# Optimization experiments

Hardware: AMD Instinct MI355X
Metric: run time of the kernel (lower is better)

Reference implementation:

```python
import jax, jax.numpy as jnp
import numpy as np

N, E, B, L, D, H = 50000, 800000, 64, 32, 256, 256


def setup_inputs() -> dict:
    key = jax.random.key(0)
    ks = jax.random.split(key, 20)
    s = 0.05
    inp = {
        'x': jax.random.normal(ks[0], (N, D), jnp.float32),
        'edge_index': jax.random.randint(ks[1], (2, E), 0, N),
        'batch': jnp.sort(jax.random.randint(ks[2], (N,), 0, B)),
        'paths': jax.random.randint(ks[3], (B, L), 0, N),
        # SAGEConv1: lin_l (aggregated neighbors, with bias) + lin_r (root, no bias)
        'w1l': jax.random.normal(ks[4], (D, H), jnp.float32) * s,
        'b1l': jnp.zeros((H,), jnp.float32),
        'w1r': jax.random.normal(ks[5], (D, H), jnp.float32) * s,
        # SAGEConv2
        'w2l': jax.random.normal(ks[6], (H, H), jnp.float32) * s,
        'b2l': jnp.zeros((H,), jnp.float32),
        'w2r': jax.random.normal(ks[7], (H, H), jnp.float32) * s,
        # LSTM (gate order i,f,g,o as in torch)
        'w_ih': jax.random.normal(ks[8], (4 * H, H), jnp.float32) * s,
        'w_hh': jax.random.normal(ks[9], (4 * H, H), jnp.float32) * s,
        'b_ih': jnp.zeros((4 * H,), jnp.float32),
        'b_hh': jnp.zeros((4 * H,), jnp.float32),
        # scorer MLP
        'wm1': jax.random.normal(ks[10], (2 * H, H), jnp.float32) * s,
        'bm1': jnp.zeros((H,), jnp.float32),
        'wm2': jax.random.normal(ks[11], (H, 1), jnp.float32) * s,
        'bm2': jnp.zeros((1,), jnp.float32),
    }
    return inp


def sage_conv(x, src, dst, wl, bl, wr):
    # mean-aggregate neighbor features (messages flow src -> dst)
    agg = jax.ops.segment_sum(x[src], dst, num_segments=N)
    deg = jax.ops.segment_sum(jnp.ones((src.shape[0],), x.dtype), dst, num_segments=N)
    mean = agg / jnp.maximum(deg, 1.0)[:, None]
    return mean @ wl + bl + x @ wr


def lstm_last_hidden(seq, w_ih, w_hh, b_ih, b_hh):
    # seq: [B, L, H] -> hn: [B, H]
    h0 = jnp.zeros((seq.shape[0], H), seq.dtype)
    c0 = jnp.zeros_like(h0)

    def step(carry, xt):
        h, c = carry
        gates = xt @ w_ih.T + b_ih + h @ w_hh.T + b_hh
        i, f, g, o = jnp.split(gates, 4, axis=-1)
        c = jax.nn.sigmoid(f) * c + jax.nn.sigmoid(i) * jnp.tanh(g)
        h = jax.nn.sigmoid(o) * jnp.tanh(c)
        return (h, c), None

    (hn, _), _ = jax.lax.scan(step, (h0, c0), jnp.swapaxes(seq, 0, 1))
    return hn


def reference(x, edge_index, batch, paths, w1l, b1l, w1r, w2l, b2l, w2r,
              w_ih, w_hh, b_ih, b_hh, wm1, bm1, wm2, bm2):
    src, dst = edge_index[0], edge_index[1]
    h = jax.nn.relu(sage_conv(x, src, dst, w1l, b1l, w1r))
    node_emb = sage_conv(h, src, dst, w2l, b2l, w2r)  # [N, H]

    # global mean pool per graph
    gsum = jax.ops.segment_sum(node_emb, batch, num_segments=B)
    gcnt = jax.ops.segment_sum(jnp.ones((N,), node_emb.dtype), batch, num_segments=B)
    graph_emb = gsum / jnp.maximum(gcnt, 1.0)[:, None]  # [B, H]

    path_seq = node_emb[paths]  # [B, L, H]
    path_emb = lstm_last_hidden(path_seq, w_ih, w_hh, b_ih, b_hh)  # [B, H]

    combined = jnp.concatenate([graph_emb, path_emb], axis=-1)  # [B, 2H]
    scores = jax.nn.relu(combined @ wm1 + bm1) @ wm2 + bm2  # [B, 1]
    return scores.reshape(-1)  # torch.cat of per-path [1] scores -> [B]
```

## Files before the change

### kernel.cpp

```cpp
#include <hip/hip_runtime.h>

namespace {

constexpr int NN = 50000;
constexpr int NE = 800000;
constexpr int NB = 64;
constexpr int NL = 32;
constexpr int ND = 256;
constexpr int NSCAN = 196;

typedef __attribute__((ext_vector_type(8))) short short8v;
typedef __attribute__((ext_vector_type(4))) float float4v;

__device__ __forceinline__ float sigf(float x){ return 1.0f/(1.0f + __expf(-x)); }

__device__ __forceinline__ void split8(float4 fa, float4 fb, uint4& h, uint4& lo){
  uint a0=__float_as_uint(fa.x), a1=__float_as_uint(fa.y), a2=__float_as_uint(fa.z), a3=__float_as_uint(fa.w);
  uint b0=__float_as_uint(fb.x), b1=__float_as_uint(fb.y), b2=__float_as_uint(fb.z), b3=__float_as_uint(fb.w);
  h.x = (a0>>16) | (a1 & 0xFFFF0000u);
  h.y = (a2>>16) | (a3 & 0xFFFF0000u);
  h.z = (b0>>16) | (b1 & 0xFFFF0000u);
  h.w = (b2>>16) | (b3 & 0xFFFF0000u);
  float r0 = fa.x - __uint_as_float(a0 & 0xFFFF0000u);
  float r1 = fa.y - __uint_as_float(a1 & 0xFFFF0000u);
  float r2 = fa.z - __uint_as_float(a2 & 0xFFFF0000u);
  float r3 = fa.w - __uint_as_float(a3 & 0xFFFF0000u);
  float r4 = fb.x - __uint_as_float(b0 & 0xFFFF0000u);
  float r5 = fb.y - __uint_as_float(b1 & 0xFFFF0000u);
  float r6 = fb.z - __uint_as_float(b2 & 0xFFFF0000u);
  float r7 = fb.w - __uint_as_float(b3 & 0xFFFF0000u);
  lo.x = (__float_as_uint(r0)>>16) | (__float_as_uint(r1) & 0xFFFF0000u);
  lo.y = (__float_as_uint(r2)>>16) | (__float_as_uint(r3) & 0xFFFF0000u);
  lo.z = (__float_as_uint(r4)>>16) | (__float_as_uint(r5) & 0xFFFF0000u);
  lo.w = (__float_as_uint(r6)>>16) | (__float_as_uint(r7) & 0xFFFF0000u);
}

__global__ void k_hist(const int* __restrict__ dst, int* __restrict__ cnt){
  int stride = gridDim.x * blockDim.x;
  for (int e = blockIdx.x*blockDim.x + threadIdx.x; e < NE; e += stride)
    atomicAdd(&cnt[dst[e]], 1);
}

__global__ void k_scan_block(const int* __restrict__ cnt, int* __restrict__ offs,
                             int* __restrict__ bsum){
  __shared__ int s[256];
  const int t = threadIdx.x, i = blockIdx.x*256 + t;
  int v = cnt[i];
  s[t] = v; __syncthreads();
  #pragma unroll
  for (int off = 1; off < 256; off <<= 1){
    int x = (t >= off) ? s[t-off] : 0;
    __syncthreads();
    s[t] += x;
    __syncthreads();
  }
  offs[i] = s[t] - v;
  if (t == 255) bsum[blockIdx.x] = s[255];
}

__global__ void k_scan_top(const int* __restrict__ bsum, int* __restrict__ bsum2){
  __shared__ int s[256];
  const int t = threadIdx.x;
  int v = (t < NSCAN) ? bsum[t] : 0;
  s[t] = v; __syncthreads();
  #pragma unroll
  for (int off = 1; off < 256; off <<= 1){
    int x = (t >= off) ? s[t-off] : 0;
    __syncthreads();
    s[t] += x;
    __syncthreads();
  }
  if (t < NSCAN) bsum2[t] = s[t] - v;
}

__global__ void k_scan_add(int* __restrict__ offs, const int* __restrict__ bsum2,
                           int* __restrict__ cursor){
  const int i = blockIdx.x*256 + threadIdx.x;
  int v = offs[i] + bsum2[blockIdx.x];
  offs[i] = v;
  cursor[i] = v;
}

__global__ void k_fill(const int* __restrict__ src, const int* __restrict__ dst,
                       int* __restrict__ cursor, int* __restrict__ csr){
  int stride = gridDim.x * blockDim.x;
  for (int e = blockIdx.x*blockDim.x + threadIdx.x; e < NE; e += stride){
    int d = dst[e];
    int pos = atomicAdd(&cursor[d], 1);
    csr[pos] = src[e];
  }
}

__launch_bounds__(256, 8)
__global__ void k_gather(const float* __restrict__ feat, const int* __restrict__ offs,
                         const int* __restrict__ csr, float* __restrict__ out){
  __shared__ float4 sp[256];
  const int u = blockIdx.x, t = threadIdx.x;
  const int w = t >> 6, l = t & 63;
  const int beg = offs[u], end = offs[u+1];
  const int lc = l * 4;
  float a0 = 0.f, a1 = 0.f, a2 = 0.f, a3 = 0.f;
  int e = beg + w;
  for (; e + 4 < end; e += 8){
    int s0 = csr[e], s1 = csr[e+4];
    const float4 v0 = *(const float4*)(feat + (long long)s0*ND + lc);
    const float4 v1 = *(const float4*)(feat + (long long)s1*ND + lc);
    a0 += v0.x + v1.x; a1 += v0.y + v1.y; a2 += v0.z + v1.z; a3 += v0.w + v1.w;
  }
  if (e < end){
    int s0 = csr[e];
    const float4 v0 = *(const float4*)(feat + (long long)s0*ND + lc);
    a0 += v0.x; a1 += v0.y; a2 += v0.z; a3 += v0.w;
  }
  sp[t] = make_float4(a0, a1, a2, a3);
  __syncthreads();
  if (t < 64){
    float4 p0 = sp[t], p1 = sp[64+t], p2 = sp[128+t], p3 = sp[192+t];
    float inv = 1.0f / fmaxf((float)(end - beg), 1.0f);
    float4 r;
    r.x = (p0.x + p1.x + p2.x + p3.x) * inv;
    r.y = (p0.y + p1.y + p2.y + p3.y) * inv;
    r.z = (p0.z + p1.z + p2.z + p3.z) * inv;
    r.w = (p0.w + p1.w + p2.w + p3.w) * inv;
    *(float4*)(out + (long long)u*ND + t*4) = r;
  }
}

__global__ void k_wsplit(const float* __restrict__ wl, const float* __restrict__ wr,
                         ushort* __restrict__ WtH, ushort* __restrict__ WtL){
  const int k = blockIdx.x;
  const int n = threadIdx.x;
  float v = (k < 256) ? wl[k*256 + n] : wr[(k-256)*256 + n];
  uint u = __float_as_uint(v);
  float r = v - __uint_as_float(u & 0xFFFF0000u);
  const int wc = n >> 6, nt = (n >> 4) & 3, lm = n & 15;
  const int kk = k >> 5, lq = (k >> 3) & 3, j = k & 7;
  const long long idx = (long long)(((wc*4 + nt)*16 + kk)*64 + lq*16 + lm)*8 + j;
  WtH[idx] = (ushort)(u >> 16);
  WtL[idx] = (ushort)(__float_as_uint(r) >> 16);
}

__launch_bounds__(256, 2)
__global__ void k_gemm_mfma(const float* __restrict__ A1, const float* __restrict__ A2,
                            const ushort* __restrict__ WtH, const ushort* __restrict__ WtL,
                            const float* __restrict__ bias, float* __restrict__ C, int relu)
{
  __shared__ float eb[16*260];
  const int t  = threadIdx.x;
  const int w  = t >> 6;
  const int l  = t & 63;
  const int lm = l & 15;
  const int lq = l >> 4;
  const int m0 = blockIdx.x * 64;

  const uint4* BH4 = (const uint4*)WtH;
  const uint4* BL4 = (const uint4*)WtL;

  const float4v vzero = {0.f, 0.f, 0.f, 0.f};
  float4v acc[4][4];
  #pragma unroll
  for (int i = 0; i < 4; ++i)
    #pragma unroll
    for (int j = 0; j < 4; ++j) acc[i][j] = vzero;

  long long arow[4];
  #pragma unroll
  for (int mt = 0; mt < 4; ++mt){
    int row = m0 + mt*16 + lm;
    row = (row < NN) ? row : (NN - 1);
    arow[mt] = (long long)row * ND;
  }
  int bbase[4];
  #pragma unroll
  for (int nt = 0; nt < 4; ++nt) bbase[nt] = (w*4 + nt)*1024 + l;

  auto ldB = [&](int kk, uint4* bh, uint4* bl){
    #pragma unroll
    for (int nt = 0; nt < 4; ++nt){
      int idx = bbase[nt] + kk*64;
      bh[nt] = BH4[idx];
      bl[nt] = BL4[idx];
    }
  };
  auto ldA = [&](int kk, uint4* ah, uint4* al){
    const float* Ab = (kk < 8) ? A1 : A2;
    const int koff = (kk & 7)*32 + lq*8;
    #pragma unroll
    for (int mt = 0; mt < 4; ++mt){
      const float* p = Ab + arow[mt] + koff;
      float4 fa = *(const float4*)p;
      float4 fb = *(const float4*)(p + 4);
      split8(fa, fb, ah[mt], al[mt]);
    }
  };

  uint4 bhb[2][4], blb[2][4], ahb[2][4], alb[2][4];
  ldB(0, bhb[0], blb[0]);
  ldA(0, ahb[0], alb[0]);

  #pragma unroll
  for (int kk = 0; kk < 16; ++kk){
    const int cur = kk & 1, nx = cur ^ 1;
    if (kk < 15){
      ldB(kk + 1, bhb[nx], blb[nx]);
      ldA(kk + 1, ahb[nx], alb[nx]);
    }
    #pragma unroll
    for (int nt = 0; nt < 4; ++nt){
      short8v bh = *(short8v*)&bhb[cur][nt];
      short8v bl = *(short8v*)&blb[cur][nt];
      #pragma unroll
      for (int mt = 0; mt < 4; ++mt){
        short8v ah = *(short8v*)&ahb[cur][mt];
        short8v al = *(short8v*)&alb[cur][mt];
        acc[mt][nt] = __builtin_amdgcn_mfma_f32_16x16x32_bf16(ah, bh, acc[mt][nt], 0, 0, 0);
        acc[mt][nt] = __builtin_amdgcn_mfma_f32_16x16x32_bf16(al, bh, acc[mt][nt], 0, 0, 0);
        acc[mt][nt] = __builtin_amdgcn_mfma_f32_16x16x32_bf16(ah, bl, acc[mt][nt], 0, 0, 0);
      }
    }
  }

  float bvv[4];
  #pragma unroll
  for (int nt = 0; nt < 4; ++nt) bvv[nt] = bias[w*64 + nt*16 + lm];

  #pragma unroll
  for (int mt = 0; mt < 4; ++mt){
    #pragma unroll
    for (int nt = 0; nt < 4; ++nt){
      #pragma unroll
      for (int r = 0; r < 4; ++r){
        float v = acc[mt][nt][r] + bvv[nt];
        if (relu) v = fmaxf(v, 0.f);
        eb[(lq*4 + r)*260 + w*64 + nt*16 + lm] = v;
      }
    }
    __syncthreads();
    #pragma unroll
    for (int i = 0; i < 4; ++i){
      int idx = i*256 + t;
      int rr  = idx >> 6;
      int c4  = (idx & 63) * 4;
      int grow = m0 + mt*16 + rr;
      if (grow < NN)
        *(float4*)(C + (long long)grow*ND + c4) = *(float4*)&eb[rr*260 + c4];
    }
    __syncthreads();
  }
}

__launch_bounds__(256, 3)
__global__ void k_xgate(const float* __restrict__ emb, const int* __restrict__ paths,
                        const float* __restrict__ w_ih, const float* __restrict__ b_ih,
                        const float* __restrict__ b_hh, float* __restrict__ xg)
{
  __shared__ float As[16][68];
  __shared__ float Ws[16][260];
  const int t  = threadIdx.x;
  const int m0 = blockIdx.x * 64;
  const int g0 = blockIdx.y * 256;
  const int rg = t >> 5, cg = t & 31;
  const int sm = t >> 2, sj = (t & 3) * 4;

  float acc[8][8];
  #pragma unroll
  for (int i = 0; i < 8; ++i)
    #pragma unroll
    for (int j = 0; j < 8; ++j) acc[i][j] = 0.f;

  const int node = paths[m0 + sm];
  const float* arow = emb  + (long long)node*ND;
  const float* wrow = w_ih + (long long)(g0 + t)*ND;

  for (int k0 = 0; k0 < 256; k0 += 16){
    float4 av = *(const float4*)(arow + k0 + sj);
    float4 q0 = *(const float4*)(wrow + k0 + 0);
    float4 q1 = *(const float4*)(wrow + k0 + 4);
    float4 q2 = *(const float4*)(wrow + k0 + 8);
    float4 q3 = *(const float4*)(wrow + k0 + 12);
    __syncthreads();
    As[sj+0][sm]=av.x; As[sj+1][sm]=av.y; As[sj+2][sm]=av.z; As[sj+3][sm]=av.w;
    Ws[ 0][t]=q0.x; Ws[ 1][t]=q0.y; Ws[ 2][t]=q0.z; Ws[ 3][t]=q0.w;
    Ws[ 4][t]=q1.x; Ws[ 5][t]=q1.y; Ws[ 6][t]=q1.z; Ws[ 7][t]=q1.w;
    Ws[ 8][t]=q2.x; Ws[ 9][t]=q2.y; Ws[10][t]=q2.z; Ws[11][t]=q2.w;
    Ws[12][t]=q3.x; Ws[13][t]=q3.y; Ws[14][t]=q3.z; Ws[15][t]=q3.w;
    __syncthreads();
    #pragma unroll
    for (int k = 0; k < 16; ++k){
      float a[8], b[8];
      *(float4*)&a[0] = *(const float4*)&As[k][rg*8];
      *(float4*)&a[4] = *(const float4*)&As[k][rg*8+4];
      *(float4*)&b[0] = *(const float4*)&Ws[k][cg*8];
      *(float4*)&b[4] = *(const float4*)&Ws[k][cg*8+4];
      #pragma unroll
      for (int i = 0; i < 8; ++i)
        #pragma unroll
        for (int j = 0; j < 8; ++j)
          acc[i][j] = fmaf(a[i], b[j], acc[i][j]);
    }
  }

  float bv[8];
  #pragma unroll
  for (int j = 0; j < 8; ++j){ int g = g0 + cg*8 + j; bv[j] = b_ih[g] + b_hh[g]; }
  #pragma unroll
  for (int i = 0; i < 8; ++i){
    int row = m0 + rg*8 + i;
    float o[8];
    #pragma unroll
    for (int j = 0; j < 8; ++j) o[j] = acc[i][j] + bv[j];
    *(float4*)(xg + (long long)row*1024 + g0 + cg*8 + 0) = *(float4*)&o[0];
    *(float4*)(xg + (long long)row*1024 + g0 + cg*8 + 4) = *(float4*)&o[4];
  }
}

__launch_bounds__(256, 4)
__global__ void k_lstm_step(const float* __restrict__ h_in, float* __restrict__ h_out,
                            float* __restrict__ c_state, const float* __restrict__ xg,
                            const float* __restrict__ w_hh, int tstep)
{
  __shared__ float ws[4*256];
  __shared__ float hs[32*260];
  __shared__ float part[2*128];
  __shared__ float gs[128];
  const int t  = threadIdx.x;
  const int u  = blockIdx.x >> 1;
  const int b0 = (blockIdx.x & 1) * 32;

  {
    int gate = t >> 6, c4 = (t & 63) * 4;
    float4 v = *(const float4*)(w_hh + (long long)(gate*256 + u)*256 + c4);
    *(float4*)&ws[gate*256 + c4] = v;
  }
  #pragma unroll
  for (int i = 0; i < 8; ++i){
    int idx = i*256 + t;
    int b = idx >> 6, c4 = (idx & 63) * 4;
    float4 v = *(const float4*)(h_in + (long long)(b0 + b)*256 + c4);
    *(float4*)&hs[b*260 + c4] = v;
  }
  __syncthreads();

  const int b  = t & 31;
  const int g  = (t >> 5) & 3;
  const int kd = t >> 7;
  float s = 0.f;
  const float* hp = &hs[b*260 + kd*128];
  const float* wp = &ws[g*256 + kd*128];
  #pragma unroll
  for (int k4 = 0; k4 < 32; ++k4){
    float4 h4 = *(const float4*)(hp + k4*4);
    float4 w4 = *(const float4*)(wp + k4*4);
    s += h4.x*w4.x + h4.y*w4.y + h4.z*w4.z + h4.w*w4.w;
  }
  part[kd*128 + b*4 + g] = s;
  __syncthreads();

  if (t < 128){
    int bb = t >> 2, gg = t & 3;
    const float* xp = xg + ((long long)(b0 + bb)*NL + tstep)*1024;
    gs[t] = part[t] + part[128 + t] + xp[gg*256 + u];
  }
  __syncthreads();

  if (t < 32){
    float gi = gs[t*4+0], gf = gs[t*4+1], gG = gs[t*4+2], go = gs[t*4+3];
    int bb = b0 + t;
    float c_old = c_state[bb*256 + u];
    float c_new = sigf(gf)*c_old + sigf(gi)*tanhf(gG);
    c_state[bb*256 + u] = c_new;
    h_out[bb*256 + u] = sigf(go)*tanhf(c_new);
  }
}

__global__ void k_pool(const float* __restrict__ emb, const int* __restrict__ batch,
                       float* __restrict__ gsum, float* __restrict__ gcnt)
{
  __shared__ int bs[256];
  const int t  = threadIdx.x;
  const int n0 = blockIdx.x * 256;
  {
    int n = n0 + t;
    bs[t] = (n < NN) ? batch[n] : -1;
  }
  __syncthreads();
  int cur = bs[0];
  float acc = 0.f; int cnt = 0;
  for (int j = 0; j < 256; ++j){
    int nn = n0 + j;
    if (nn >= NN) break;
    int g = bs[j];
    if (g != cur){
      unsafeAtomicAdd(&gsum[cur*256 + t], acc);
      if (t == 0) unsafeAtomicAdd(&gcnt[cur], (float)cnt);
      acc = 0.f; cnt = 0; cur = g;
    }
    acc += emb[(long long)nn*256 + t];
    ++cnt;
  }
  if (cnt > 0 && cur >= 0){
    unsafeAtomicAdd(&gsum[cur*256 + t], acc);
    if (t == 0) unsafeAtomicAdd(&gcnt[cur], (float)cnt);
  }
}

__global__ void k_score(const float* __restrict__ gsum, const float* __restrict__ gcnt,
                        const float* __restrict__ hfin, const float* __restrict__ wm1,
                        const float* __restrict__ bm1, const float* __restrict__ wm2,
                        const float* __restrict__ bm2, float* __restrict__ out)
{
  __shared__ float cs[512];
  __shared__ float red[4];
  const int b = blockIdx.x, t = threadIdx.x;
  float inv = 1.0f / fmaxf(gcnt[b], 1.0f);
  cs[t]       = gsum[b*256 + t] * inv;
  cs[256 + t] = hfin[b*256 + t];
  __syncthreads();
  float v = 0.f;
  #pragma unroll 4
  for (int k = 0; k < 512; ++k) v = fmaf(cs[k], wm1[(long long)k*256 + t], v);
  v = fmaxf(v + bm1[t], 0.f) * wm2[t];
  #pragma unroll
  for (int off = 32; off > 0; off >>= 1) v += __shfl_down(v, off, 64);
  if ((t & 63) == 0) red[t >> 6] = v;
  __syncthreads();
  if (t == 0) out[b] = red[0] + red[1] + red[2] + red[3] + bm2[0];
}

}

extern "C" void kernel_launch(void* const* d_in, const int* in_sizes, int n_in,
                              void* d_out, int out_size, void* d_ws, size_t ws_size,
                              hipStream_t stream)
{
  const float* x     = (const float*)d_in[0];
  const int*   eidx  = (const int*)  d_in[1];
  const int*   batch = (const int*)  d_in[2];
  const int*   paths = (const int*)  d_in[3];
  const float* w1l   = (const float*)d_in[4];
  const float* b1l   = (const float*)d_in[5];
  const float* w1r   = (const float*)d_in[6];
  const float* w2l   = (const float*)d_in[7];
  const float* b2l   = (const float*)d_in[8];
  const float* w2r   = (const float*)d_in[9];
  const float* w_ih  = (const float*)d_in[10];
  const float* w_hh  = (const float*)d_in[11];
  const float* b_ih  = (const float*)d_in[12];
  const float* b_hh  = (const float*)d_in[13];
  const float* wm1   = (const float*)d_in[14];
  const float* bm1   = (const float*)d_in[15];
  const float* wm2   = (const float*)d_in[16];
  const float* bm2   = (const float*)d_in[17];

  const int* src = eidx;
  const int* dst = eidx + NE;

  float* w    = (float*)d_ws;
  float* bufA = w;
  float* bufB = bufA + (long long)NN*ND;
  float* xg   = bufB + (long long)NN*ND;
  float* gsum = xg   + 2048*1024;
  float* gcnt = gsum + NB*ND;
  float* h0   = gcnt + 64;
  float* c0   = h0   + NB*ND;
  float* h1   = c0   + NB*ND;
  ushort* wt1H = (ushort*)(h1 + NB*ND);
  ushort* wt1L = wt1H + 256*512;
  ushort* wt2H = wt1L + 256*512;
  ushort* wt2L = wt2H + 256*512;

  int* cnt    = (int*)xg;
  int* offs   = cnt    + 50432;
  int* cursor = offs   + 50432;
  int* bsum   = cursor + 50432;
  int* bsum2  = bsum   + 256;
  int* csr    = bsum2  + 256;

  k_wsplit<<<512, 256, 0, stream>>>(w1l, w1r, wt1H, wt1L);
  k_wsplit<<<512, 256, 0, stream>>>(w2l, w2r, wt2H, wt2L);

  hipMemsetAsync(cnt, 0, 50432*sizeof(int), stream);
  k_hist<<<1024, 256, 0, stream>>>(dst, cnt);
  k_scan_block<<<NSCAN, 256, 0, stream>>>(cnt, offs, bsum);
  k_scan_top<<<1, 256, 0, stream>>>(bsum, bsum2);
  k_scan_add<<<NSCAN, 256, 0, stream>>>(offs, bsum2, cursor);
  k_fill<<<1024, 256, 0, stream>>>(src, dst, cursor, csr);

  k_gather<<<NN, 256, 0, stream>>>(x, offs, csr, bufA);
  k_gemm_mfma<<<(NN+63)/64, 256, 0, stream>>>(bufA, x, wt1H, wt1L, b1l, bufB, 1);

  k_gather<<<NN, 256, 0, stream>>>(bufB, offs, csr, bufA);
  k_gemm_mfma<<<(NN+63)/64, 256, 0, stream>>>(bufA, bufB, wt2H, wt2L, b2l, bufA, 0);

  hipMemsetAsync(gsum, 0, (NB*ND + 64)*sizeof(float), stream);
  k_pool<<<(NN+255)/256, 256, 0, stream>>>(bufA, batch, gsum, gcnt);

  k_xgate<<<dim3((NB*NL)/64, 1024/256), 256, 0, stream>>>(bufA, paths, w_ih, b_ih, b_hh, xg);

  hipMemsetAsync(h0, 0, 2*(size_t)NB*ND*sizeof(float), stream);
  for (int ts = 0; ts < NL; ++ts){
    float* hin  = (ts & 1) ? h1 : h0;
    float* hout = (ts & 1) ? h0 : h1;
    k_lstm_step<<<512, 256, 0, stream>>>(hin, hout, c0, xg, w_hh, ts);
  }

  k_score<<<NB, 256, 0, stream>>>(gsum, gcnt, h0, wm1, bm1, wm2, bm2, (float*)d_out);
}
```

Before: 941.6 us.

## Fuse LSTM timesteps into one cooperative persistent kernel with split-bf16 MFMA

Replaces the 32 per-timestep LSTM kernel launches with a single cooperative kernel of 64 blocks. Each block keeps its slice of w_hh in shared memory as hi/lo bf16 pairs and computes the recurrent matvec with three bf16 MFMAs per k-step. Timesteps are separated by a grid-wide sync, and the cell state stays in registers. This removes per-step launch overhead and the repeated reload of w_hh, in exchange for grid barrier latency and a small precision loss from the bf16 split.

```diff
diff --git a/kernel.cpp b/kernel.cpp
--- a/kernel.cpp
+++ b/kernel.cpp
@@ -1,4 +1,7 @@
 #include <hip/hip_runtime.h>
+#include <hip/hip_cooperative_groups.h>
+
+namespace cg = cooperative_groups;
 
 namespace {
 
@@ -314,62 +317,94 @@
   }
 }
 
-__launch_bounds__(256, 4)
-__global__ void k_lstm_step(const float* __restrict__ h_in, float* __restrict__ h_out,
-                            float* __restrict__ c_state, const float* __restrict__ xg,
-                            const float* __restrict__ w_hh, int tstep)
+__launch_bounds__(256, 1)
+__global__ void k_lstm(const float* __restrict__ xg, const float* __restrict__ w_hh,
+                       ushort* __restrict__ hH, ushort* __restrict__ hL,
+                       float* __restrict__ hfin)
 {
-  __shared__ float ws[4*256];
-  __shared__ float hs[32*260];
-  __shared__ float part[2*128];
-  __shared__ float gs[128];
+  cg::grid_group grid = cg::this_grid();
+  __shared__ ushort Bh[8*64*8];
+  __shared__ ushort Bl[8*64*8];
+  __shared__ float  Gs[4*256];
   const int t  = threadIdx.x;
-  const int u  = blockIdx.x >> 1;
-  const int b0 = (blockIdx.x & 1) * 32;
-
-  {
-    int gate = t >> 6, c4 = (t & 63) * 4;
-    float4 v = *(const float4*)(w_hh + (long long)(gate*256 + u)*256 + c4);
-    *(float4*)&ws[gate*256 + c4] = v;
-  }
-  #pragma unroll
-  for (int i = 0; i < 8; ++i){
-    int idx = i*256 + t;
-    int b = idx >> 6, c4 = (idx & 63) * 4;
-    float4 v = *(const float4*)(h_in + (long long)(b0 + b)*256 + c4);
-    *(float4*)&hs[b*260 + c4] = v;
+  const int w  = t >> 6, l = t & 63;
+  const int b  = blockIdx.x;
+  const int u0 = b*4;
+  const int lm = l & 15, lq = l >> 4;
+  const int m0w = w*16;
+
+  #pragma unroll
+  for (int i = 0; i < 16; ++i){
+    int elem = i*256 + t;
+    int n = elem >> 8;
+    int k = elem & 255;
+    float v = w_hh[((n >> 2)*256 + u0 + (n & 3))*256 + k];
+    uint uv = __float_as_uint(v);
+    float r = v - __uint_as_float(uv & 0xFFFF0000u);
+    int kk = k >> 5, lqq = (k >> 3) & 3, jj = k & 7;
+    int pos = (kk*64 + lqq*16 + n)*8 + jj;
+    Bh[pos] = (ushort)(uv >> 16);
+    Bl[pos] = (ushort)(__float_as_uint(r) >> 16);
   }
   __syncthreads();
 
-  const int b  = t & 31;
-  const int g  = (t >> 5) & 3;
-  const int kd = t >> 7;
-  float s = 0.f;
-  const float* hp = &hs[b*260 + kd*128];
-  const float* wp = &ws[g*256 + kd*128];
-  #pragma unroll
-  for (int k4 = 0; k4 < 32; ++k4){
-    float4 h4 = *(const float4*)(hp + k4*4);
-    float4 w4 = *(const float4*)(wp + k4*4);
-    s += h4.x*w4.x + h4.y*w4.y + h4.z*w4.z + h4.w*w4.w;
-  }
-  part[kd*128 + b*4 + g] = s;
-  __syncthreads();
-
-  if (t < 128){
-    int bb = t >> 2, gg = t & 3;
-    const float* xp = xg + ((long long)(b0 + bb)*NL + tstep)*1024;
-    gs[t] = part[t] + part[128 + t] + xp[gg*256 + u];
-  }
-  __syncthreads();
-
-  if (t < 32){
-    float gi = gs[t*4+0], gf = gs[t*4+1], gG = gs[t*4+2], go = gs[t*4+3];
-    int bb = b0 + t;
-    float c_old = c_state[bb*256 + u];
-    float c_new = sigf(gf)*c_old + sigf(gi)*tanhf(gG);
-    c_state[bb*256 + u] = c_new;
-    h_out[bb*256 + u] = sigf(go)*tanhf(c_new);
+  const int mb = m0w + lm;
+  const int uu = u0 + lq;
+  float c = 0.f;
+
+  float xq[4];
+  #pragma unroll
+  for (int g = 0; g < 4; ++g) xq[g] = xg[(mb*NL + 0)*1024 + g*256 + uu];
+
+  for (int ts = 0; ts < NL; ++ts){
+    const int tsn = (ts < NL-1) ? ts + 1 : ts;
+    float xqn[4];
+    #pragma unroll
+    for (int g = 0; g < 4; ++g) xqn[g] = xg[(mb*NL + tsn)*1024 + g*256 + uu];
+
+    if (ts > 0){
+      const ushort* hHp = hH + ((ts-1) & 1)*16384;
+      const ushort* hLp = hL + ((ts-1) & 1)*16384;
+      float4v acc = {0.f, 0.f, 0.f, 0.f};
+      #pragma unroll
+      for (int kk = 0; kk < 8; ++kk){
+        const int koff = kk*32 + lq*8;
+        short8v ah = *(const short8v*)(hHp + mb*256 + koff);
+        short8v al = *(const short8v*)(hLp + mb*256 + koff);
+        short8v bh = *(const short8v*)&Bh[(kk*64 + l)*8];
+        short8v bl = *(const short8v*)&Bl[(kk*64 + l)*8];
+        acc = __builtin_amdgcn_mfma_f32_16x16x32_bf16(ah, bh, acc, 0, 0, 0);
+        acc = __builtin_amdgcn_mfma_f32_16x16x32_bf16(al, bh, acc, 0, 0, 0);
+        acc = __builtin_amdgcn_mfma_f32_16x16x32_bf16(ah, bl, acc, 0, 0, 0);
+      }
+      #pragma unroll
+      for (int r = 0; r < 4; ++r)
+        Gs[w*256 + (lq*4 + r)*16 + lm] = acc[r];
+    } else {
+      #pragma unroll
+      for (int r = 0; r < 4; ++r)
+        Gs[w*256 + (lq*4 + r)*16 + lm] = 0.f;
+    }
+    __syncthreads();
+
+    float gi = Gs[w*256 + lm*16 +  0 + lq] + xq[0];
+    float gf = Gs[w*256 + lm*16 +  4 + lq] + xq[1];
+    float gg = Gs[w*256 + lm*16 +  8 + lq] + xq[2];
+    float go = Gs[w*256 + lm*16 + 12 + lq] + xq[3];
+    float c_new = sigf(gf)*c + sigf(gi)*tanhf(gg);
+    c = c_new;
+    float h = sigf(go)*tanhf(c_new);
+
+    uint hu = __float_as_uint(h);
+    float hr = h - __uint_as_float(hu & 0xFFFF0000u);
+    hH[(ts & 1)*16384 + mb*256 + uu] = (ushort)(hu >> 16);
+    hL[(ts & 1)*16384 + mb*256 + uu] = (ushort)(__float_as_uint(hr) >> 16);
+    if (ts == NL-1) hfin[mb*256 + uu] = h;
+
+    xq[0]=xqn[0]; xq[1]=xqn[1]; xq[2]=xqn[2]; xq[3]=xqn[3];
+    __threadfence();
+    grid.sync();
+    __syncthreads();
   }
 }
 
@@ -462,12 +497,12 @@
   float* gsum = xg   + 2048*1024;
   float* gcnt = gsum + NB*ND;
   float* h0   = gcnt + 64;
-  float* c0   = h0   + NB*ND;
-  float* h1   = c0   + NB*ND;
-  ushort* wt1H = (ushort*)(h1 + NB*ND);
+  ushort* wt1H = (ushort*)(h0 + NB*ND);
   ushort* wt1L = wt1H + 256*512;
   ushort* wt2H = wt1L + 256*512;
   ushort* wt2L = wt2H + 256*512;
+  ushort* hH   = wt2L + 256*512;
+  ushort* hL   = hH   + 2*NB*ND;
 
   int* cnt    = (int*)xg;
   int* offs   = cnt    + 50432;
@@ -497,11 +532,12 @@
 
   k_xgate<<<dim3((NB*NL)/64, 1024/256), 256, 0, stream>>>(bufA, paths, w_ih, b_ih, b_hh, xg);
 
-  hipMemsetAsync(h0, 0, 2*(size_t)NB*ND*sizeof(float), stream);
-  for (int ts = 0; ts < NL; ++ts){
-    float* hin  = (ts & 1) ? h1 : h0;
-    float* hout = (ts & 1) ? h0 : h1;
-    k_lstm_step<<<512, 256, 0, stream>>>(hin, hout, c0, xg, w_hh, ts);
+  {
+    const float* xg_c = xg;
+    const float* whh_c = w_hh;
+    ushort* hH_c = hH; ushort* hL_c = hL; float* h0_c = h0;
+    void* args[] = { (void*)&xg_c, (void*)&whh_c, (void*)&hH_c, (void*)&hL_c, (void*)&h0_c };
+    hipLaunchCooperativeKernel((const void*)k_lstm, dim3(64), dim3(256), args, 0, stream);
   }
 
   k_score<<<NB, 256, 0, stream>>>(gsum, gcnt, h0, wm1, bm1, wm2, bm2, (float*)d_out);
```

New measurement: 1.451 ms. +54.1%, slower.

## Gather neighbor features from bf16 copies to halve gather traffic

Applied to the files above, without the earlier changes.

Adds a kernel that converts x to bf16 with round-to-nearest-even, and makes the first GEMM also write a bf16 copy of its ReLU output. Both neighbor-mean gathers now read bf16 rows and accumulate in fp32. The aim is to halve the bytes moved by the random-access gather, which reads about 800k rows of 1KB each per layer. In exchange it adds a conversion pass and an extra bf16 write, and the aggregated neighbor features lose precision.

```diff
diff --git a/kernel.cpp b/kernel.cpp
--- a/kernel.cpp
+++ b/kernel.cpp
@@ -13,6 +13,12 @@
 typedef __attribute__((ext_vector_type(4))) float float4v;
 
 __device__ __forceinline__ float sigf(float x){ return 1.0f/(1.0f + __expf(-x)); }
+
+__device__ __forceinline__ ushort rne_bf16(float f){
+  uint u = __float_as_uint(f);
+  return (ushort)((u + 0x7FFFu + ((u >> 16) & 1u)) >> 16);
+}
+__device__ __forceinline__ float bf2f(ushort u){ return __uint_as_float((uint)u << 16); }
 
 __device__ __forceinline__ void split8(float4 fa, float4 fb, uint4& h, uint4& lo){
   uint a0=__float_as_uint(fa.x), a1=__float_as_uint(fa.y), a2=__float_as_uint(fa.z), a3=__float_as_uint(fa.w);
@@ -91,9 +97,18 @@
   }
 }
 
+__global__ void k_tobf16(const float* __restrict__ in, ushort* __restrict__ out){
+  const int i = blockIdx.x*blockDim.x + threadIdx.x;
+  const float4 a = ((const float4*)in)[i*2];
+  const float4 b = ((const float4*)in)[i*2+1];
+  ushort o[8] = { rne_bf16(a.x), rne_bf16(a.y), rne_bf16(a.z), rne_bf16(a.w),
+                  rne_bf16(b.x), rne_bf16(b.y), rne_bf16(b.z), rne_bf16(b.w) };
+  ((uint4*)out)[i] = *(uint4*)o;
+}
+
 __launch_bounds__(256, 8)
-__global__ void k_gather(const float* __restrict__ feat, const int* __restrict__ offs,
-                         const int* __restrict__ csr, float* __restrict__ out){
+__global__ void k_gather_bf16(const ushort* __restrict__ feat, const int* __restrict__ offs,
+                              const int* __restrict__ csr, float* __restrict__ out){
   __shared__ float4 sp[256];
   const int u = blockIdx.x, t = threadIdx.x;
   const int w = t >> 6, l = t & 63;
@@ -103,14 +118,17 @@
   int e = beg + w;
   for (; e + 4 < end; e += 8){
     int s0 = csr[e], s1 = csr[e+4];
-    const float4 v0 = *(const float4*)(feat + (long long)s0*ND + lc);
-    const float4 v1 = *(const float4*)(feat + (long long)s1*ND + lc);
-    a0 += v0.x + v1.x; a1 += v0.y + v1.y; a2 += v0.z + v1.z; a3 += v0.w + v1.w;
+    ushort4 v0 = *(const ushort4*)(feat + (long long)s0*ND + lc);
+    ushort4 v1 = *(const ushort4*)(feat + (long long)s1*ND + lc);
+    a0 += bf2f(v0.x) + bf2f(v1.x);
+    a1 += bf2f(v0.y) + bf2f(v1.y);
+    a2 += bf2f(v0.z) + bf2f(v1.z);
+    a3 += bf2f(v0.w) + bf2f(v1.w);
   }
   if (e < end){
     int s0 = csr[e];
-    const float4 v0 = *(const float4*)(feat + (long long)s0*ND + lc);
-    a0 += v0.x; a1 += v0.y; a2 += v0.z; a3 += v0.w;
+    ushort4 v0 = *(const ushort4*)(feat + (long long)s0*ND + lc);
+    a0 += bf2f(v0.x); a1 += bf2f(v0.y); a2 += bf2f(v0.z); a3 += bf2f(v0.w);
   }
   sp[t] = make_float4(a0, a1, a2, a3);
   __syncthreads();
@@ -143,7 +161,8 @@
 __launch_bounds__(256, 2)
 __global__ void k_gemm_mfma(const float* __restrict__ A1, const float* __restrict__ A2,
                             const ushort* __restrict__ WtH, const ushort* __restrict__ WtL,
-                            const float* __restrict__ bias, float* __restrict__ C, int relu)
+                            const float* __restrict__ bias, float* __restrict__ C,
+                            ushort* __restrict__ Cb, int relu)
 {
   __shared__ float eb[16*260];
   const int t  = threadIdx.x;
@@ -242,8 +261,14 @@
       int rr  = idx >> 6;
       int c4  = (idx & 63) * 4;
       int grow = m0 + mt*16 + rr;
-      if (grow < NN)
-        *(float4*)(C + (long long)grow*ND + c4) = *(float4*)&eb[rr*260 + c4];
+      if (grow < NN){
+        float4 fv = *(float4*)&eb[rr*260 + c4];
+        *(float4*)(C + (long long)grow*ND + c4) = fv;
+        if (Cb){
+          ushort ub[4] = { rne_bf16(fv.x), rne_bf16(fv.y), rne_bf16(fv.z), rne_bf16(fv.w) };
+          *(ushort4*)(Cb + (long long)grow*ND + c4) = *(ushort4*)ub;
+        }
+      }
     }
     __syncthreads();
   }
@@ -468,6 +493,7 @@
   ushort* wt1L = wt1H + 256*512;
   ushort* wt2H = wt1L + 256*512;
   ushort* wt2L = wt2H + 256*512;
+  ushort* fb16 = wt2L + 256*512;
 
   int* cnt    = (int*)xg;
   int* offs   = cnt    + 50432;
@@ -479,6 +505,8 @@
   k_wsplit<<<512, 256, 0, stream>>>(w1l, w1r, wt1H, wt1L);
   k_wsplit<<<512, 256, 0, stream>>>(w2l, w2r, wt2H, wt2L);
 
+  k_tobf16<<<(NN*ND/8 + 255)/256, 256, 0, stream>>>(x, fb16);
+
   hipMemsetAsync(cnt, 0, 50432*sizeof(int), stream);
   k_hist<<<1024, 256, 0, stream>>>(dst, cnt);
   k_scan_block<<<NSCAN, 256, 0, stream>>>(cnt, offs, bsum);
@@ -486,11 +514,11 @@
   k_scan_add<<<NSCAN, 256, 0, stream>>>(offs, bsum2, cursor);
   k_fill<<<1024, 256, 0, stream>>>(src, dst, cursor, csr);
 
-  k_gather<<<NN, 256, 0, stream>>>(x, offs, csr, bufA);
-  k_gemm_mfma<<<(NN+63)/64, 256, 0, stream>>>(bufA, x, wt1H, wt1L, b1l, bufB, 1);
-
-  k_gather<<<NN, 256, 0, stream>>>(bufB, offs, csr, bufA);
-  k_gemm_mfma<<<(NN+63)/64, 256, 0, stream>>>(bufA, bufB, wt2H, wt2L, b2l, bufA, 0);
+  k_gather_bf16<<<NN, 256, 0, stream>>>(fb16, offs, csr, bufA);
+  k_gemm_mfma<<<(NN+63)/64, 256, 0, stream>>>(bufA, x, wt1H, wt1L, b1l, bufB, fb16, 1);
+
+  k_gather_bf16<<<NN, 256, 0, stream>>>(fb16, offs, csr, bufA);
+  k_gemm_mfma<<<(NN+63)/64, 256, 0, stream>>>(bufA, bufB, wt2H, wt2L, b2l, bufA, (ushort*)nullptr, 0);
 
   hipMemsetAsync(gsum, 0, (NB*ND + 64)*sizeof(float), stream);
   k_pool<<<(NN+255)/256, 256, 0, stream>>>(bufA, batch, gsum, gcnt);
```

Result: faster. 872.2 us (-7.4%).
